# Optimization experiments

Hardware: AMD Instinct MI355X
Metric: run time of the kernel (lower is better)

## Reference

```python
import jax, jax.numpy as jnp
import numpy as np

T, N, E = 4, 50000, 800000
F, H, C_HID, C_OUT = 256, 128, 512, 2
SLOPE = 11.0 / 48.0  # torch RReLU eval-mode slope = (1/8 + 1/3) / 2


def _topk_pool(x, scorer, k):
    # x: [N, d], scorer: [d, 1] -> [d, k]
    scores = (x @ scorer) / jnp.maximum(jnp.linalg.norm(scorer), 1e-6)  # [N, 1]
    _, idx = jax.lax.top_k(scores[:, 0], k)
    return (x[idx] * jnp.tanh(scores[idx])).T


def _gru_cell(prev_Q, z, Wu, Uu, bu, Wr, Ur, br, Wh, Uh, bh):
    u = jax.nn.sigmoid(Wu @ z + Uu @ prev_Q + bu)
    r = jax.nn.sigmoid(Wr @ z + Ur @ prev_Q + br)
    h_cap = jnp.tanh(Wh @ z + Uh @ (r * prev_Q) + bh)
    return (1.0 - u) * prev_Q + u * h_cap


def _gcn_conv(x, src, dst, W):
    ones = jnp.ones(src.shape[0], x.dtype)
    deg_out = jnp.clip(jax.ops.segment_sum(ones, src, num_segments=N), 1.0)
    deg_in = jnp.clip(jax.ops.segment_sum(ones, dst, num_segments=N), 1.0)
    h = (x * (deg_out ** -0.5)[:, None]) @ W          # project first (out <= in)
    agg = jax.ops.segment_sum(h[src], dst, num_segments=N)
    out = agg * (deg_in ** -0.5)[:, None]
    return jnp.where(out >= 0, out, SLOPE * out)      # RReLU (eval mode)


def setup_inputs() -> dict:
    key = jax.random.key(0)
    ks = jax.random.split(key, 32)
    s = 0.05
    d = {}
    d['feats'] = jax.random.normal(ks[0], (T, N, F), jnp.float32)
    d['edges'] = jax.random.randint(ks[1], (T, 2, E), 0, N)
    d['scorer0'] = jax.random.normal(ks[2], (F, 1), jnp.float32) * s
    d['scorer1'] = jax.random.normal(ks[3], (H, 1), jnp.float32) * s
    d['gcn_W0'] = jax.random.normal(ks[4], (F, H), jnp.float32) * s
    d['gcn_W1'] = jax.random.normal(ks[5], (H, H), jnp.float32) * s
    i = 6
    for g in ('u', 'r', 'h'):
        d[g + '_W0'] = jax.random.normal(ks[i], (F, F), jnp.float32) * s; i += 1
        d[g + '_U0'] = jax.random.normal(ks[i], (F, F), jnp.float32) * s; i += 1
        d[g + '_b0'] = jax.random.normal(ks[i], (F, H), jnp.float32) * s; i += 1
    for g in ('u', 'r', 'h'):
        d[g + '_W1'] = jax.random.normal(ks[i], (H, H), jnp.float32) * s; i += 1
        d[g + '_U1'] = jax.random.normal(ks[i], (H, H), jnp.float32) * s; i += 1
        d[g + '_b1'] = jax.random.normal(ks[i], (H, H), jnp.float32) * s; i += 1
    d['mlp_W1'] = jax.random.normal(ks[i], (H, C_HID), jnp.float32) * s; i += 1
    d['mlp_b1'] = jax.random.normal(ks[i], (C_HID,), jnp.float32) * s; i += 1
    d['mlp_W2'] = jax.random.normal(ks[i], (C_HID, C_OUT), jnp.float32) * s; i += 1
    d['mlp_b2'] = jax.random.normal(ks[i], (C_OUT,), jnp.float32) * s
    return d


def reference(feats, edges, scorer0, scorer1, gcn_W0, gcn_W1,
              u_W0, u_U0, u_b0, r_W0, r_U0, r_b0, h_W0, h_U0, h_b0,
              u_W1, u_U1, u_b1, r_W1, r_U1, r_b1, h_W1, h_U1, h_b1,
              mlp_W1, mlp_b1, mlp_W2, mlp_b2):
    feat_list = [feats[t] for t in range(T)]
    scorers = [scorer0, scorer1]
    gcn_Ws = [gcn_W0, gcn_W1]
    grus = [(u_W0, u_U0, u_b0, r_W0, r_U0, r_b0, h_W0, h_U0, h_b0),
            (u_W1, u_U1, u_b1, r_W1, r_U1, r_b1, h_W1, h_U1, h_b1)]
    for i in range(2):
        W = gcn_Ws[i]
        for t in range(T):
            src, dst = edges[t, 0], edges[t, 1]
            X_tilde = _topk_pool(feat_list[t], scorers[i], H)
            W = _gru_cell(W, X_tilde, *grus[i])
            feat_list[t] = _gcn_conv(feat_list[t], src, dst, W)
    x = feat_list[-1]
    x = jnp.maximum(x @ mlp_W1 + mlp_b1, 0.0)
    return x @ mlp_W2 + mlp_b2
```

## Files before the change

kernel.cpp:

```cpp
#include <hip/hip_runtime.h>

#define NT 4
#define NN 50000
#define NE 800000
#define FD 256
#define HD 128
#define CH 512
#define NBINS 4096
#define CAPC 256
#define RSLOPE 0.22916666666666666f

#define NCH 32
#define CHE (NE / NCH)
#define HALFN 25000
#define WPH 12500
#define WPC 25000

#define C_NORM0 0
#define C_NORM1 1

#define SCAN_BLOCKS 49
#define BT0SZ (HD * 2 * FD)
#define BT1SZ (HD * 2 * HD)

typedef __attribute__((ext_vector_type(8))) short bf16x8;
typedef __attribute__((ext_vector_type(4))) float f32x4;

__device__ __forceinline__ float wsumf(float v) {
  for (int m = 32; m > 0; m >>= 1) v += __shfl_xor(v, m, 64);
  return v;
}

__device__ __forceinline__ unsigned short f2bf(float x) {
  unsigned int u = __float_as_uint(x);
  u += 0x7fffu + ((u >> 16) & 1u);
  return (unsigned short)(u >> 16);
}
__device__ __forceinline__ float bf2f(unsigned short h) {
  return __uint_as_float(((unsigned int)h) << 16);
}
__device__ __forceinline__ int sbin(float s) {
  int b = (int)floorf((s + 16.f) * 128.f);
  return max(0, min(NBINS - 1, b));
}

__global__ void k_norm(const float* __restrict__ s, int d, float* ctlf, int slot) {
  __shared__ float red[256];
  float v = ((int)threadIdx.x < d) ? s[threadIdx.x] * s[threadIdx.x] : 0.f;
  red[threadIdx.x] = v;
  __syncthreads();
  for (int o = 128; o > 0; o >>= 1) {
    if ((int)threadIdx.x < o) red[threadIdx.x] += red[threadIdx.x + o];
    __syncthreads();
  }
  if (threadIdx.x == 0) ctlf[slot] = fmaxf(sqrtf(red[0]), 1e-6f);
}

__global__ __launch_bounds__(1024) void k_degC(const int* __restrict__ edges,
                                               unsigned int* __restrict__ chist) {
  __shared__ unsigned int lcnt[WPH];
  int t = blockIdx.y, c = blockIdx.x;
  int tid = threadIdx.x;
  for (int dir = 0; dir < 2; ++dir) {
    const int* E = edges + (size_t)t * 2 * NE + (size_t)dir * NE + (size_t)c * CHE;
    for (int half = 0; half < 2; ++half) {
      for (int i = tid; i < WPH; i += 1024) lcnt[i] = 0;
      __syncthreads();
      int lo = half * HALFN;
      for (int j = tid; j < CHE; j += 1024) {
        int n = E[j] - lo;
        if ((unsigned)n < (unsigned)HALFN)
          atomicAdd(&lcnt[n >> 1], 1u << ((n & 1) * 16));
      }
      __syncthreads();
      unsigned int* dst = chist + (((size_t)dir * NT + t) * NCH + c) * WPC + (size_t)half * WPH;
      for (int i = tid; i < WPH; i += 1024) dst[i] = lcnt[i];
      __syncthreads();
    }
  }
}

__global__ __launch_bounds__(1024) void k_scanB(const unsigned int* __restrict__ chist,
                                                unsigned int* __restrict__ lbase,
                                                float* __restrict__ dor4,
                                                float* __restrict__ din4,
                                                int* __restrict__ rowptr4,
                                                int* __restrict__ bsum4) {
  int t = blockIdx.y;
// ... 76 lines not shown
  const int* rowptr = rowptr4 + (size_t)t * (NN + 1);
  const unsigned int* lb = lbase + ((size_t)t * NCH + c) * NN;
  int* srcs = srcs4 + (size_t)t * NE;
  for (int half = 0; half < 2; ++half) {
    for (int i = tid; i < WPH; i += 1024) lcnt[i] = 0;
    __syncthreads();
    int lo = half * HALFN;
    for (int j = tid; j < CHE; j += 1024) {
      int d = dstE[j];
      int n = d - lo;
      if ((unsigned)n < (unsigned)HALFN) {
        unsigned int old = atomicAdd(&lcnt[n >> 1], 1u << ((n & 1) * 16));
        int ord = (int)((old >> ((n & 1) * 16)) & 0xffff);
        int pos = rowptr[d] + (int)lb[d] + ord;
        srcs[pos] = srcE[j];
      }
    }
    __syncthreads();
  }
}

__global__ void k_scores0_all(const float* __restrict__ feats, const float* __restrict__ sc,
                              const float* __restrict__ ctlf, float* __restrict__ scores0) {
  int t = blockIdx.y;
  int w = (blockIdx.x * blockDim.x + threadIdx.x) >> 6;
  int lane = threadIdx.x & 63;
  if (w >= NN) return;
  size_t rowoff = ((size_t)t * NN + w) * FD;
  float4 x = *(const float4*)(feats + rowoff + lane * 4);
  float4 s = *(const float4*)(sc + lane * 4);
  double acc = (double)x.x * s.x + (double)x.y * s.y + (double)x.z * s.z + (double)x.w * s.w;
  for (int m = 32; m > 0; m >>= 1) acc += __shfl_xor(acc, m, 64);
  if (lane == 0) scores0[(size_t)t * NN + w] = (float)(acc / (double)ctlf[C_NORM0]);
}

__global__ __launch_bounds__(256) void k_cvtT(const float* __restrict__ src, int R, int C,
                                              unsigned short* __restrict__ dhi,
                                              unsigned short* __restrict__ dlo,
                                              int ldd, int roff) {
  __shared__ float t[32][33];
  int bc = blockIdx.x * 32, br = blockIdx.y * 32;
  int lr = threadIdx.x >> 5, lc = threadIdx.x & 31;
#pragma unroll
  for (int q = 0; q < 4; ++q) {
    int r = br + lr + q * 8;
    t[lr + q * 8][lc] = src[(size_t)r * C + bc + lc];
  }
  __syncthreads();
#pragma unroll
  for (int q = 0; q < 4; ++q) {
    int dr = lr + q * 8;
    float v = t[lc][dr];
    unsigned short h = f2bf(v);
    unsigned short l = f2bf(v - bf2f(h));
    size_t o = (size_t)(bc + dr) * ldd + roff + br + lc;
    dhi[o] = h;
    dlo[o] = l;
  }
}

__global__ void k_catsplit(int d, const float* __restrict__ Wu, const float* __restrict__ Uu,
                           const float* __restrict__ Wr, const float* __restrict__ Ur,
                           const float* __restrict__ Wh,
                           unsigned short* __restrict__ hi, unsigned short* __restrict__ lo) {
  int idx = blockIdx.x * 256 + threadIdx.x;
  int K = 2 * d;
  if (idx >= 3 * d * K) return;
  int row = idx / K, col = idx - row * K;
  int reg = row / d;
  int i = row - reg * d;
  float v;
  if (reg == 0) v = (col < d) ? Wu[i * d + col] : Uu[i * d + col - d];
  else if (reg == 1) v = (col < d) ? Wr[i * d + col] : Ur[i * d + col - d];
  else v = (col < d) ? Wh[i * d + col] : 0.f;
  unsigned short h = f2bf(v);
  hi[idx] = h;
  lo[idx] = f2bf(v - bf2f(h));
}

__global__ void k_split(int n, const float* __restrict__ src,
                        unsigned short* __restrict__ hi, unsigned short* __restrict__ lo) {
  int idx = blockIdx.x * 256 + threadIdx.x;
  if (idx >= n) return;
  float v = src[idx];
  unsigned short h = f2bf(v);
  hi[idx] = h;
  lo[idx] = f2bf(v - bf2f(h));
}

template <int LOGD>
__global__ __launch_bounds__(1024) void k_pool(const float* __restrict__ Xb, long xStride,
                                               const float* __restrict__ scoresB, int sStride,
                                               unsigned short* __restrict__ bthiB,
                                               unsigned short* __restrict__ btloB,
                                               long btStride, int ldb) {
  const int D = 1 << LOGD;
  int t = blockIdx.x;
  const float* X = Xb + (size_t)t * xStride;
  const float* scores = scoresB + (size_t)t * sStride;
  unsigned short* bthi = bthiB + (size_t)t * btStride;
  unsigned short* btlo = btloB + (size_t)t * btStride;
  __shared__ int hist[NBINS];
  __shared__ int sufT[1024];
  __shared__ float cs[CAPC];
  __shared__ int ci[CAPC];
  __shared__ float stv[HD];
  __shared__ int sidx[HD];
  __shared__ int thrBin, cnt;
  int tid = threadIdx.x;
  for (int i = tid; i < NBINS; i += 1024) hist[i] = 0;
  if (tid == 0) cnt = 0;
  __syncthreads();
  for (int i = tid; i < NN; i += 1024) atomicAdd(&hist[sbin(scores[i])], 1);
  __syncthreads();

  int h0 = hist[4 * tid + 0], h1 = hist[4 * tid + 1];
  int h2 = hist[4 * tid + 2], h3 = hist[4 * tid + 3];
  int l3 = h3, l2 = h2 + l3, l1 = h1 + l2, l0 = h0 + l1;
  sufT[tid] = l0;
  __syncthreads();
// ... 35 lines not shown
          float si = cs[i], sl = cs[l];
          int di = ci[i], dl = ci[l];
          bool lb = (sl > si) || (sl == si && dl < di);
          bool ib = (si > sl) || (si == sl && di < dl);
          bool dir = ((i & k) == 0);
          if (dir ? lb : ib) {
            cs[i] = sl; cs[l] = si; ci[i] = dl; ci[l] = di;
          }
        }
      }
      __syncthreads();
    }
  }
  if (tid < HD) {
    stv[tid] = tanhf(cs[tid]);
    sidx[tid] = ci[tid];
  }
  __syncthreads();
  for (int e4 = tid * 4; e4 < D * HD; e4 += 1024 * 4) {
    int j = e4 >> LOGD, f = e4 & (D - 1);
    float4 x = *(const float4*)&X[(size_t)sidx[j] * D + f];
    float sv = stv[j];
    x.x *= sv; x.y *= sv; x.z *= sv; x.w *= sv;
    ushort4 h, l;
    h.x = f2bf(x.x); l.x = f2bf(x.x - bf2f(h.x));
    h.y = f2bf(x.y); l.y = f2bf(x.y - bf2f(h.y));
    h.z = f2bf(x.z); l.z = f2bf(x.z - bf2f(h.z));
    h.w = f2bf(x.w); l.w = f2bf(x.w - bf2f(h.w));
    *(ushort4*)&bthi[(size_t)j * ldb + f] = h;
    *(ushort4*)&btlo[(size_t)j * ldb + f] = l;
  }
}

__global__ __launch_bounds__(256) void k_gruA(
    const unsigned short* __restrict__ Ahi, const unsigned short* __restrict__ Alo,
    const unsigned short* __restrict__ Bhi, const unsigned short* __restrict__ Blo,
    int d, const float* __restrict__ bu, const float* __restrict__ br,
    const float* __restrict__ bh, const float* __restrict__ Q,
    float* __restrict__ u, float* __restrict__ hz,
    unsigned short* __restrict__ rqThi, unsigned short* __restrict__ rqTlo) {
  __shared__ unsigned short AshH[64 * 32], AshL[64 * 32];
  __shared__ unsigned short BshH[128 * 32], BshL[128 * 32];
  int K = 2 * d;
  int tid = threadIdx.x;
  int lane = tid & 63, wave = tid >> 6;
  int wr = wave >> 1, wc = wave & 1;
  int n0 = blockIdx.x * 64;
  f32x4 acc[2][4];
#pragma unroll
  for (int m = 0; m < 2; ++m)
#pragma unroll
    for (int n = 0; n < 4; ++n) acc[m][n] = (f32x4){0.f, 0.f, 0.f, 0.f};
  int arow = tid >> 2, aseg = tid & 3;
  int as = (aseg ^ (arow & 3)) * 8;
  int kseg = lane >> 4;
  for (int k0 = 0; k0 < K; k0 += 32) {
    __syncthreads();
    {
      size_t off = (size_t)(n0 + arow) * K + k0 + aseg * 8;
      *(bf16x8*)&AshH[arow * 32 + as] = *(const bf16x8*)(Ahi + off);
      *(bf16x8*)&AshL[arow * 32 + as] = *(const bf16x8*)(Alo + off);
    }
#pragma unroll
    for (int h = 0; h < 2; ++h) {
      int id = tid + h * 256;
      int br2 = id >> 2, bseg = id & 3;
      int bs = (bseg ^ (br2 & 3)) * 8;
      size_t off = (size_t)br2 * K + k0 + bseg * 8;
      *(bf16x8*)&BshH[br2 * 32 + bs] = *(const bf16x8*)(Bhi + off);
      *(bf16x8*)&BshL[br2 * 32 + bs] = *(const bf16x8*)(Blo + off);
    }
    __syncthreads();
    bf16x8 ah[2], al[2], bh8[4], bl8[4];
#pragma unroll
    for (int m = 0; m < 2; ++m) {
      int row = wr * 32 + m * 16 + (lane & 15);
      int s = (kseg ^ (row & 3)) * 8;
      ah[m] = *(bf16x8*)&AshH[row * 32 + s];
      al[m] = *(bf16x8*)&AshL[row * 32 + s];
    }
// ... 10 lines not shown
      for (int n = 0; n < 4; ++n) {
        acc[m][n] = __builtin_amdgcn_mfma_f32_16x16x32_bf16(ah[m], bh8[n], acc[m][n], 0, 0, 0);
        acc[m][n] = __builtin_amdgcn_mfma_f32_16x16x32_bf16(al[m], bh8[n], acc[m][n], 0, 0, 0);
        acc[m][n] = __builtin_amdgcn_mfma_f32_16x16x32_bf16(ah[m], bl8[n], acc[m][n], 0, 0, 0);
      }
  }
  int reg = n0 / d;
#pragma unroll
  for (int m = 0; m < 2; ++m) {
#pragma unroll
    for (int q = 0; q < 4; ++q) {
      int row = n0 + wr * 32 + m * 16 + (lane >> 4) * 4 + q;
      int i = row - reg * d;
#pragma unroll
      for (int n = 0; n < 4; ++n) {
        int col = wc * 64 + n * 16 + (lane & 15);
        float a = acc[m][n][q];
        if (reg == 0) {
          u[i * HD + col] = 1.f / (1.f + expf(-(a + bu[i * HD + col])));
        } else if (reg == 1) {
          float r = 1.f / (1.f + expf(-(a + br[i * HD + col])));
          float rq = r * Q[i * HD + col];
          unsigned short h = f2bf(rq);
          rqThi[(size_t)col * d + i] = h;
          rqTlo[(size_t)col * d + i] = f2bf(rq - bf2f(h));
        } else {
          hz[i * HD + col] = a + bh[i * HD + col];
        }
      }
    }
  }
}

__global__ __launch_bounds__(256) void k_gruB(
    const unsigned short* __restrict__ Ahi, const unsigned short* __restrict__ Alo,
    const unsigned short* __restrict__ Bhi, const unsigned short* __restrict__ Blo,
    int d, const float* __restrict__ hz, const float* __restrict__ u,
    float* __restrict__ Q, unsigned short* __restrict__ BTWhi,
    unsigned short* __restrict__ BTWlo, int ldbt) {
  __shared__ unsigned short AshH[64 * 32], AshL[64 * 32];
  __shared__ unsigned short BshH[128 * 32], BshL[128 * 32];
  int K = d;
  int tid = threadIdx.x;
  int lane = tid & 63, wave = tid >> 6;
  int wr = wave >> 1, wc = wave & 1;
  int n0 = blockIdx.x * 64;
  f32x4 acc[2][4];
#pragma unroll
  for (int m = 0; m < 2; ++m)
#pragma unroll
    for (int n = 0; n < 4; ++n) acc[m][n] = (f32x4){0.f, 0.f, 0.f, 0.f};
  int arow = tid >> 2, aseg = tid & 3;
  int as = (aseg ^ (arow & 3)) * 8;
  int kseg = lane >> 4;
  for (int k0 = 0; k0 < K; k0 += 32) {
    __syncthreads();
    {
      size_t off = (size_t)(n0 + arow) * K + k0 + aseg * 8;
      *(bf16x8*)&AshH[arow * 32 + as] = *(const bf16x8*)(Ahi + off);
      *(bf16x8*)&AshL[arow * 32 + as] = *(const bf16x8*)(Alo + off);
    }
#pragma unroll
    for (int h = 0; h < 2; ++h) {
      int id = tid + h * 256;
      int br2 = id >> 2, bseg = id & 3;
      int bs = (bseg ^ (br2 & 3)) * 8;
      size_t off = (size_t)br2 * K + k0 + bseg * 8;
      *(bf16x8*)&BshH[br2 * 32 + bs] = *(const bf16x8*)(Bhi + off);
      *(bf16x8*)&BshL[br2 * 32 + bs] = *(const bf16x8*)(Blo + off);
    }
    __syncthreads();
    bf16x8 ah[2], al[2], bh8[4], bl8[4];
#pragma unroll
    for (int m = 0; m < 2; ++m) {
      int row = wr * 32 + m * 16 + (lane & 15);
      int s = (kseg ^ (row & 3)) * 8;
      ah[m] = *(bf16x8*)&AshH[row * 32 + s];
      al[m] = *(bf16x8*)&AshL[row * 32 + s];
    }
// ... 1 lines not shown
    for (int n = 0; n < 4; ++n) {
      int col = wc * 64 + n * 16 + (lane & 15);
      int s = (kseg ^ (col & 3)) * 8;
      bh8[n] = *(bf16x8*)&BshH[col * 32 + s];
      bl8[n] = *(bf16x8*)&BshL[col * 32 + s];
    }
#pragma unroll
    for (int m = 0; m < 2; ++m)
#pragma unroll
      for (int n = 0; n < 4; ++n) {
        acc[m][n] = __builtin_amdgcn_mfma_f32_16x16x32_bf16(ah[m], bh8[n], acc[m][n], 0, 0, 0);
        acc[m][n] = __builtin_amdgcn_mfma_f32_16x16x32_bf16(al[m], bh8[n], acc[m][n], 0, 0, 0);
        acc[m][n] = __builtin_amdgcn_mfma_f32_16x16x32_bf16(ah[m], bl8[n], acc[m][n], 0, 0, 0);
      }
  }
#pragma unroll
  for (int m = 0; m < 2; ++m) {
#pragma unroll
    for (int q = 0; q < 4; ++q) {
      int i = n0 + wr * 32 + m * 16 + (lane >> 4) * 4 + q;
#pragma unroll
      for (int n = 0; n < 4; ++n) {
        int col = wc * 64 + n * 16 + (lane & 15);
        float hc = tanhf(acc[m][n][q] + hz[i * HD + col]);
        float uu = u[i * HD + col];
        float qv = Q[i * HD + col];
        float wn = (1.f - uu) * qv + uu * hc;
        Q[i * HD + col] = wn;
        unsigned short h = f2bf(wn);
        BTWhi[(size_t)col * ldbt + i] = h;
        BTWlo[(size_t)col * ldbt + i] = f2bf(wn - bf2f(h));
      }
    }
  }
}

__global__ __launch_bounds__(256) void k_convL0(
    const float* __restrict__ feats,
    const unsigned short* __restrict__ bt0hi, const unsigned short* __restrict__ bt0lo,
    float* __restrict__ C4, const float* __restrict__ dor4) {
  __shared__ unsigned short AshH[64 * 32], AshL[64 * 32];
  __shared__ unsigned short BshH[128 * 32], BshL[128 * 32];
  const int K = FD, ldb = 2 * FD;
  int t = blockIdx.z;
  const float* Af = feats + (size_t)t * NN * FD;
  size_t bOff = (size_t)((t + 1) & 3) * BT0SZ + FD;
  const unsigned short* Bhi = bt0hi + bOff;
  const unsigned short* Blo = bt0lo + bOff;
  float* C = C4 + (size_t)t * NN * HD;
  const float* rs = dor4 + (size_t)t * NN;
  int tid = threadIdx.x;
  int lane = tid & 63, wave = tid >> 6;
  int wr = wave >> 1, wc = wave & 1;
  int n0 = blockIdx.x * 64;
  f32x4 acc[2][4];
#pragma unroll
  for (int m = 0; m < 2; ++m)
#pragma unroll
    for (int n = 0; n < 4; ++n) acc[m][n] = (f32x4){0.f, 0.f, 0.f, 0.f};

  int arow = tid >> 2, aseg = tid & 3;
  int as = (aseg ^ (arow & 3)) * 8;
  int kseg = lane >> 4;

  for (int k0 = 0; k0 < K; k0 += 32) {
    __syncthreads();
// ... 124 lines not shown
#pragma unroll
    for (int n = 0; n < 4; ++n) {
      int col = wc * 64 + n * 16 + (lane & 15);
      int s = (kseg ^ (col & 3)) * 8;
      bh[n] = *(bf16x8*)&BshH[col * 32 + s];
      bl[n] = *(bf16x8*)&BshL[col * 32 + s];
    }
#pragma unroll
    for (int m = 0; m < 2; ++m)
#pragma unroll
      for (int n = 0; n < 4; ++n) {
        acc[m][n] = __builtin_amdgcn_mfma_f32_16x16x32_bf16(ah[m], bh[n], acc[m][n], 0, 0, 0);
        acc[m][n] = __builtin_amdgcn_mfma_f32_16x16x32_bf16(al[m], bh[n], acc[m][n], 0, 0, 0);
        acc[m][n] = __builtin_amdgcn_mfma_f32_16x16x32_bf16(ah[m], bl[n], acc[m][n], 0, 0, 0);
      }
  }

#pragma unroll
  for (int m = 0; m < 2; ++m) {
#pragma unroll
    for (int q = 0; q < 4; ++q) {
      int row = n0 + wr * 32 + m * 16 + (lane >> 4) * 4 + q;
      if (row >= M) continue;
      float rsv = rs[row];
#pragma unroll
      for (int n = 0; n < 4; ++n) {
        int col = c0 + wc * 64 + n * 16 + (lane & 15);
        C[(size_t)row * ldo + col] = acc[m][n][q] * rsv;
      }
    }
  }
}

__global__ __launch_bounds__(256) void k_gemmMLP(
    const unsigned short* __restrict__ Ahi, const unsigned short* __restrict__ Alo,
    const unsigned short* __restrict__ Bhi, const unsigned short* __restrict__ Blo,
    const float* __restrict__ bias, const float* __restrict__ W2,
    const float* __restrict__ b2, float* __restrict__ out, int M) {
  __shared__ unsigned short AshH[64 * 128], AshL[64 * 128];
  __shared__ unsigned short BshH[128 * 32], BshL[128 * 32];
  __shared__ float osum[64][2];
  int tid = threadIdx.x;
  int lane = tid & 63, wave = tid >> 6;
  int wr = wave >> 1, wc = wave & 1;
  int n0 = blockIdx.x * 64;
  if (tid < 128) ((float*)osum)[tid] = 0.f;

  {
    int row = tid >> 2, sq = tid & 3;
    int grow = n0 + row;
#pragma unroll
    for (int q = 0; q < 4; ++q) {
      int s = sq * 4 + q;
      bf16x8 vh = (bf16x8)(short)0, vl = (bf16x8)(short)0;
      if (grow < M) {
        size_t off = (size_t)grow * HD + s * 8;
        vh = *(const bf16x8*)(Ahi + off);
        vl = *(const bf16x8*)(Alo + off);
      }
      int sp = (s ^ (row & 15)) * 8;
      *(bf16x8*)&AshH[row * 128 + sp] = vh;
      *(bf16x8*)&AshL[row * 128 + sp] = vl;
    }
  }
  __syncthreads();

  float ps0[2][4], ps1[2][4];
#pragma unroll
  for (int m = 0; m < 2; ++m)
#pragma unroll
    for (int q = 0; q < 4; ++q) { ps0[m][q] = 0.f; ps1[m][q] = 0.f; }

  int kseg = lane >> 4;
  for (int hc = 0; hc < 4; ++hc) {
    f32x4 acc[2][4];
#pragma unroll
    for (int m = 0; m < 2; ++m)
#pragma unroll
      for (int n = 0; n < 4; ++n) acc[m][n] = (f32x4){0.f, 0.f, 0.f, 0.f};
    for (int k0 = 0; k0 < HD; k0 += 32) {
      __syncthreads();
#pragma unroll
      for (int h = 0; h < 2; ++h) {
        int id = tid + h * 256;
        int br = id >> 2, bseg = id & 3;
        int bs = (bseg ^ (br & 3)) * 8;
        size_t off = (size_t)(hc * 128 + br) * HD + k0 + bseg * 8;
        *(bf16x8*)&BshH[br * 32 + bs] = *(const bf16x8*)(Bhi + off);
        *(bf16x8*)&BshL[br * 32 + bs] = *(const bf16x8*)(Blo + off);
      }
      __syncthreads();
      bf16x8 ah[2], al[2], bh[4], bl[4];
#pragma unroll
      for (int m = 0; m < 2; ++m) {
        int row = wr * 32 + m * 16 + (lane & 15);
        int sg = (k0 >> 3) + kseg;
        int sp = (sg ^ (row & 15)) * 8;
        ah[m] = *(bf16x8*)&AshH[row * 128 + sp];
        al[m] = *(bf16x8*)&AshL[row * 128 + sp];
      }
#pragma unroll
      for (int n = 0; n < 4; ++n) {
        int col = wc * 64 + n * 16 + (lane & 15);
        int s = (kseg ^ (col & 3)) * 8;
        bh[n] = *(bf16x8*)&BshH[col * 32 + s];
        bl[n] = *(bf16x8*)&BshL[col * 32 + s];
      }
#pragma unroll
      for (int m = 0; m < 2; ++m)
#pragma unroll
        for (int n = 0; n < 4; ++n) {
          acc[m][n] = __builtin_amdgcn_mfma_f32_16x16x32_bf16(ah[m], bh[n], acc[m][n], 0, 0, 0);
          acc[m][n] = __builtin_amdgcn_mfma_f32_16x16x32_bf16(al[m], bh[n], acc[m][n], 0, 0, 0);
          acc[m][n] = __builtin_amdgcn_mfma_f32_16x16x32_bf16(ah[m], bl[n], acc[m][n], 0, 0, 0);
        }
    }
#pragma unroll
// ... 62 lines not shown
    float2 v4 = *(const float2*)&h[(size_t)s4 * HD + l2o];
    float2 v5 = *(const float2*)&h[(size_t)s5 * HD + l2o];
    float2 v6 = *(const float2*)&h[(size_t)s6 * HD + l2o];
    float2 v7 = *(const float2*)&h[(size_t)s7 * HD + l2o];
    ax += ((v0.x + v1.x) + (v2.x + v3.x)) + ((v4.x + v5.x) + (v6.x + v7.x));
    ay += ((v0.y + v1.y) + (v2.y + v3.y)) + ((v4.y + v5.y) + (v6.y + v7.y));
  }
  for (; e + 2 <= end; e += 2) {
    int s0 = srcs[e + 0], s1 = srcs[e + 1];
    float2 v0 = *(const float2*)&h[(size_t)s0 * HD + l2o];
    float2 v1 = *(const float2*)&h[(size_t)s1 * HD + l2o];
    ax += v0.x + v1.x;
    ay += v0.y + v1.y;
  }
  for (; e < end; ++e) {
    int s = srcs[e];
    float2 v = *(const float2*)&h[(size_t)s * HD + l2o];
    ax += v.x; ay += v.y;
  }
  float dn = din4[(size_t)t * NN + w];
  ax *= dn; ay *= dn;
  ax = ax >= 0.f ? ax : RSLOPE * ax;
  ay = ay >= 0.f ? ay : RSLOPE * ay;
  *(float2*)&featA4[((size_t)t * NN + w) * HD + l2o] = make_float2(ax, ay);
  if (t == NT - 1) {
    unsigned short hx = f2bf(ax), hy = f2bf(ay);
    unsigned short lx = f2bf(ax - bf2f(hx)), ly = f2bf(ay - bf2f(hy));
    *(ushort2*)&outHi[(size_t)w * HD + l2o] = make_ushort2(hx, hy);
    *(ushort2*)&outLo[(size_t)w * HD + l2o] = make_ushort2(lx, ly);
  }
  float sp = ax * scorer[l2o] + ay * scorer[l2o + 1];
  sp = wsumf(sp);
  if (lane == 0) scores1_4[(size_t)t * NN + w] = sp / ctlf[C_NORM1];
}

__global__ void k_aggF(const float* __restrict__ h, const int* __restrict__ rowptr,
                       const int* __restrict__ srcs, const float* __restrict__ din,
                       unsigned short* __restrict__ outHi, unsigned short* __restrict__ outLo) {
  int w = (blockIdx.x * blockDim.x + threadIdx.x) >> 6;
  int lane = threadIdx.x & 63;
  if (w >= NN) return;
  int beg = rowptr[w], end = rowptr[w + 1];
  float ax = 0.f, ay = 0.f;
  int e = beg;
  int l2o = lane * 2;
  for (; e + 8 <= end; e += 8) {
    int s0 = srcs[e + 0], s1 = srcs[e + 1], s2 = srcs[e + 2], s3 = srcs[e + 3];
    int s4 = srcs[e + 4], s5 = srcs[e + 5], s6 = srcs[e + 6], s7 = srcs[e + 7];
    float2 v0 = *(const float2*)&h[(size_t)s0 * HD + l2o];
    float2 v1 = *(const float2*)&h[(size_t)s1 * HD + l2o];
    float2 v2 = *(const float2*)&h[(size_t)s2 * HD + l2o];
    float2 v3 = *(const float2*)&h[(size_t)s3 * HD + l2o];
    float2 v4 = *(const float2*)&h[(size_t)s4 * HD + l2o];
    float2 v5 = *(const float2*)&h[(size_t)s5 * HD + l2o];
    float2 v6 = *(const float2*)&h[(size_t)s6 * HD + l2o];
    float2 v7 = *(const float2*)&h[(size_t)s7 * HD + l2o];
    ax += ((v0.x + v1.x) + (v2.x + v3.x)) + ((v4.x + v5.x) + (v6.x + v7.x));
    ay += ((v0.y + v1.y) + (v2.y + v3.y)) + ((v4.y + v5.y) + (v6.y + v7.y));
  }
  for (; e + 2 <= end; e += 2) {
    int s0 = srcs[e + 0], s1 = srcs[e + 1];
    float2 v0 = *(const float2*)&h[(size_t)s0 * HD + l2o];
    float2 v1 = *(const float2*)&h[(size_t)s1 * HD + l2o];
    ax += v0.x + v1.x;
    ay += v0.y + v1.y;
  }
  for (; e < end; ++e) {
    int s = srcs[e];
    float2 v = *(const float2*)&h[(size_t)s * HD + l2o];
    ax += v.x; ay += v.y;
  }
  float dn = din[w];
  ax *= dn; ay *= dn;
  ax = ax >= 0.f ? ax : RSLOPE * ax;
  ay = ay >= 0.f ? ay : RSLOPE * ay;
  unsigned short hx = f2bf(ax), hy = f2bf(ay);
  unsigned short lx = f2bf(ax - bf2f(hx)), ly = f2bf(ay - bf2f(hy));
  *(ushort2*)&outHi[(size_t)w * HD + l2o] = make_ushort2(hx, hy);
  *(ushort2*)&outLo[(size_t)w * HD + l2o] = make_ushort2(lx, ly);
}

extern "C" void kernel_launch(void* const* d_in, const int* in_sizes, int n_in,
                              void* d_out, int out_size, void* d_ws, size_t ws_size,
                              hipStream_t stream) {
  (void)in_sizes; (void)n_in; (void)out_size; (void)ws_size;
  const float* feats = (const float*)d_in[0];
  const int* edges = (const int*)d_in[1];
  const float* scorer0 = (const float*)d_in[2];
  const float* scorer1 = (const float*)d_in[3];
  const float* gcnW0 = (const float*)d_in[4];
  const float* gcnW1 = (const float*)d_in[5];
  const float* g0[9];
  const float* g1[9];
  for (int i = 0; i < 9; ++i) {
    g0[i] = (const float*)d_in[6 + i];
    g1[i] = (const float*)d_in[15 + i];
  }
  const float* mlpW1 = (const float*)d_in[24];
  const float* mlpB1 = (const float*)d_in[25];
  const float* mlpW2 = (const float*)d_in[26];
  const float* mlpB2 = (const float*)d_in[27];
  float* out = (float*)d_out;

  char* p = (char*)d_ws;
  auto carve = [&p](size_t bytes) {
    void* r = (void*)p;
    p += (bytes + 511) & ~(size_t)511;
    return r;
  };
  float* featA4 = (float*)carve((size_t)NT * NN * HD * 4);
  float* hbuf4  = (float*)carve((size_t)NT * NN * HD * 4);
  unsigned short* fahi = (unsigned short*)carve((size_t)NN * HD * 2);
  unsigned short* falo = (unsigned short*)carve((size_t)NN * HD * 2);
  int* srcs4   = (int*)carve((size_t)NT * NE * 4);
  int* rowptr4 = (int*)carve((size_t)NT * (NN + 1) * 4);
  unsigned int* chist = (unsigned int*)carve((size_t)2 * NT * NCH * WPC * 4);
  unsigned int* lbase = (unsigned int*)carve((size_t)NT * NCH * NN * 4);
  int* bsum4   = (int*)carve((size_t)NT * SCAN_BLOCKS * 4);
  float* dor4  = (float*)carve((size_t)NT * NN * 4);
  float* din4  = (float*)carve((size_t)NT * NN * 4);
  float* scores0 = (float*)carve((size_t)NT * NN * 4);
  float* scores1_4 = (float*)carve((size_t)NT * NN * 4);
  float* ctlf  = (float*)carve(64 * 4);
  unsigned short* bt0hi = (unsigned short*)carve((size_t)NT * BT0SZ * 2);
  unsigned short* bt0lo = (unsigned short*)carve((size_t)NT * BT0SZ * 2);
  unsigned short* bt1hi = (unsigned short*)carve((size_t)NT * BT1SZ * 2);
  unsigned short* bt1lo = (unsigned short*)carve((size_t)NT * BT1SZ * 2);
  unsigned short* rqThi = (unsigned short*)carve((size_t)HD * FD * 2);
  unsigned short* rqTlo = (unsigned short*)carve((size_t)HD * FD * 2);
  float* ubuf_f = (float*)carve((size_t)FD * HD * 4);
  float* hzbuf  = (float*)carve((size_t)FD * HD * 4);
  unsigned short* acat0hi = (unsigned short*)carve((size_t)3 * FD * 2 * FD * 2);
  unsigned short* acat0lo = (unsigned short*)carve((size_t)3 * FD * 2 * FD * 2);
  unsigned short* acat1hi = (unsigned short*)carve((size_t)3 * HD * 2 * HD * 2);
  unsigned short* acat1lo = (unsigned short*)carve((size_t)3 * HD * 2 * HD * 2);
  unsigned short* uh0hi = (unsigned short*)carve((size_t)FD * FD * 2);
  unsigned short* uh0lo = (unsigned short*)carve((size_t)FD * FD * 2);
  unsigned short* uh1hi = (unsigned short*)carve((size_t)HD * HD * 2);
  unsigned short* uh1lo = (unsigned short*)carve((size_t)HD * HD * 2);
  float* Q0 = (float*)carve((size_t)FD * HD * 4);
  float* Q1 = (float*)carve((size_t)HD * HD * 4);
  unsigned short* mW1thi = (unsigned short*)carve((size_t)CH * HD * 2);
  unsigned short* mW1tlo = (unsigned short*)carve((size_t)CH * HD * 2);

  hipMemcpyAsync(Q0, gcnW0, (size_t)FD * HD * 4, hipMemcpyDeviceToDevice, stream);
  hipMemcpyAsync(Q1, gcnW1, (size_t)HD * HD * 4, hipMemcpyDeviceToDevice, stream);
  k_norm<<<1, 256, 0, stream>>>(scorer0, FD, ctlf, C_NORM0);
  k_norm<<<1, 256, 0, stream>>>(scorer1, HD, ctlf, C_NORM1);
  k_cvtT<<<dim3(CH / 32, HD / 32), 256, 0, stream>>>(mlpW1, HD, CH, mW1thi, mW1tlo, HD, 0);
  k_cvtT<<<dim3(HD / 32, FD / 32), 256, 0, stream>>>(gcnW0, FD, HD, bt0hi, bt0lo, 2 * FD, FD);
  k_cvtT<<<dim3(HD / 32, HD / 32), 256, 0, stream>>>(gcnW1, HD, HD, bt1hi, bt1lo, 2 * HD, HD);
  k_catsplit<<<(3 * FD * 2 * FD + 255) / 256, 256, 0, stream>>>(FD, g0[0], g0[1], g0[3], g0[4], g0[6], acat0hi, acat0lo);
  k_catsplit<<<(3 * HD * 2 * HD + 255) / 256, 256, 0, stream>>>(HD, g1[0], g1[1], g1[3], g1[4], g1[6], acat1hi, acat1lo);
  k_split<<<(FD * FD + 255) / 256, 256, 0, stream>>>(FD * FD, g0[7], uh0hi, uh0lo);
  k_split<<<(HD * HD + 255) / 256, 256, 0, stream>>>(HD * HD, g1[7], uh1hi, uh1lo);

  k_scores0_all<<<dim3(12500, NT), 256, 0, stream>>>(feats, scorer0, ctlf, scores0);
  k_degC<<<dim3(NCH, NT), 1024, 0, stream>>>(edges, chist);
  k_scanB<<<dim3(SCAN_BLOCKS, NT), 1024, 0, stream>>>(chist, lbase, dor4, din4, rowptr4, bsum4);
  k_scan2b<<<NT, 1024, 0, stream>>>(rowptr4, bsum4);
  k_scatC<<<dim3(NCH, NT), 1024, 0, stream>>>(edges, rowptr4, lbase, srcs4);
  k_pool<8><<<NT, 1024, 0, stream>>>(feats, (long)NN * FD, scores0, NN,
                                     bt0hi, bt0lo, (long)BT0SZ, 2 * FD);

  for (int t = 0; t < NT; ++t) {
    size_t btOff = (size_t)t * BT0SZ;
    size_t btNxt = (size_t)((t + 1) & 3) * BT0SZ;
    k_gruA<<<3 * FD / 64, 256, 0, stream>>>(acat0hi, acat0lo, bt0hi + btOff, bt0lo + btOff,
                                            FD, g0[2], g0[5], g0[8], Q0, ubuf_f, hzbuf,
                                            rqThi, rqTlo);
    k_gruB<<<FD / 64, 256, 0, stream>>>(uh0hi, uh0lo, rqThi, rqTlo, FD, hzbuf, ubuf_f, Q0,
                                        bt0hi + btNxt + FD, bt0lo + btNxt + FD, 2 * FD);
  }

  const int gM = (NN + 63) / 64;

  k_convL0<<<dim3(gM, 1, NT), 256, 0, stream>>>(feats, bt0hi, bt0lo, hbuf4, dor4);

  k_aggB<<<dim3(12500, NT), 256, 0, stream>>>(hbuf4, rowptr4, srcs4, din4, featA4,
                                              scorer1, ctlf, scores1_4, fahi, falo);

  k_pool<7><<<NT, 1024, 0, stream>>>(featA4, (long)NN * HD, scores1_4, NN,
                                     bt1hi, bt1lo, (long)BT1SZ, 2 * HD);

  for (int t = 0; t < NT; ++t) {
    size_t btOff = (size_t)t * BT1SZ;
    size_t btNxt = (size_t)((t + 1) & 3) * BT1SZ;
    k_gruA<<<3 * HD / 64, 256, 0, stream>>>(acat1hi, acat1lo, bt1hi + btOff, bt1lo + btOff,
                                            HD, g1[2], g1[5], g1[8], Q1, ubuf_f, hzbuf,
                                            rqThi, rqTlo);
    k_gruB<<<HD / 64, 256, 0, stream>>>(uh1hi, uh1lo, rqThi, rqTlo, HD, hzbuf, ubuf_f, Q1,
                                        bt1hi + btNxt + HD, bt1lo + btNxt + HD, 2 * HD);
  }

  k_gemm3<<<dim3(gM, 1), 256, 0, stream>>>(fahi, falo, HD,
                                           bt1hi + HD, bt1lo + HD, 2 * HD,
                                           hbuf4, HD, NN, HD, dor4 + (size_t)3 * NN);
  k_aggF<<<12500, 256, 0, stream>>>(hbuf4, rowptr4 + (size_t)3 * (NN + 1),
                                    srcs4 + (size_t)3 * NE, din4 + (size_t)3 * NN,
                                    fahi, falo);
  k_gemmMLP<<<gM, 256, 0, stream>>>(fahi, falo, mW1thi, mW1tlo, mlpB1, mlpW2, mlpB2, out, NN);
}
```

Measured before the change: 1.089 ms.

## Merge setup kernels, run GRU chain persistently with grid barriers, fuse final aggregation into MLP

The separate setup launches and two memcpys are merged into a single k_startup kernel that dispatches on block index. Each GRU time loop is now one persistent kernel that uses a global atomic barrier between the gruA and gruB phases, replacing eight small launches per layer. The final edge aggregation is folded into the MLP GEMM's A-tile load, so the bf16 feature round trip through memory is gone. The risks are that the spin barrier assumes all blocks are co-resident, and that aggregation with one thread per 32-column segment may gather less efficiently than the old wave-per-row layout.

```diff
diff --git a/kernel.cpp b/kernel.cpp
--- a/kernel.cpp
+++ b/kernel.cpp
@@ -23,6 +23,20 @@
 #define BT0SZ (HD * 2 * FD)
 #define BT1SZ (HD * 2 * HD)
 
+#define SU_NORM0 0
+#define SU_NORM1 1
+#define SU_CVT_A 2
+#define SU_CVT_B 66
+#define SU_CVT_C 98
+#define SU_CAT0 114
+#define SU_CAT1 1650
+#define SU_SPL0 2034
+#define SU_SPL1 2290
+#define SU_CPQ0 2354
+#define SU_CPQ1 2386
+#define SU_ZBAR 2402
+#define SU_TOTAL 2403
+
 typedef __attribute__((ext_vector_type(8))) short bf16x8;
 typedef __attribute__((ext_vector_type(4))) float f32x4;
 
@@ -44,8 +58,20 @@
   return max(0, min(NBINS - 1, b));
 }
 
-__global__ void k_norm(const float* __restrict__ s, int d, float* ctlf, int slot) {
-  __shared__ float red[256];
+__device__ __forceinline__ void gbar(unsigned int* bar, int nblk, int gen) {
+  __syncthreads();
+  if (threadIdx.x == 0) {
+    __threadfence();
+    atomicAdd(bar, 1u);
+    unsigned int tgt = (unsigned int)(nblk * (gen + 1));
+    while (atomicAdd(bar, 0u) < tgt) __builtin_amdgcn_s_sleep(2);
+    __threadfence();
+  }
+  __syncthreads();
+}
+
+__device__ __forceinline__ void d_norm(const float* s, int d, float* ctlf, int slot,
+                                       float* red) {
   float v = ((int)threadIdx.x < d) ? s[threadIdx.x] * s[threadIdx.x] : 0.f;
   red[threadIdx.x] = v;
   __syncthreads();
@@ -54,6 +80,102 @@
     __syncthreads();
   }
   if (threadIdx.x == 0) ctlf[slot] = fmaxf(sqrtf(red[0]), 1e-6f);
+}
+
+__device__ __forceinline__ void d_cvtT(int bx, int by, const float* __restrict__ src, int C,
+                                       unsigned short* __restrict__ dhi,
+                                       unsigned short* __restrict__ dlo,
+                                       int ldd, int roff, float (*t)[33]) {
+  int bc = bx * 32, br = by * 32;
+  int lr = threadIdx.x >> 5, lc = threadIdx.x & 31;
+#pragma unroll
+  for (int q = 0; q < 4; ++q) {
+    int r = br + lr + q * 8;
+    t[lr + q * 8][lc] = src[(size_t)r * C + bc + lc];
+  }
+  __syncthreads();
+#pragma unroll
+  for (int q = 0; q < 4; ++q) {
+    int dr = lr + q * 8;
+    float v = t[lc][dr];
+    unsigned short h = f2bf(v);
+    unsigned short l = f2bf(v - bf2f(h));
+    size_t o = (size_t)(bc + dr) * ldd + roff + br + lc;
+    dhi[o] = h;
+    dlo[o] = l;
+  }
+}
+
+__device__ __forceinline__ void d_catsplit(int blk, int d, const float* __restrict__ Wu,
+                                           const float* __restrict__ Uu,
+                                           const float* __restrict__ Wr,
+                                           const float* __restrict__ Ur,
+                                           const float* __restrict__ Wh,
+                                           unsigned short* __restrict__ hi,
+                                           unsigned short* __restrict__ lo) {
+  int idx = blk * 256 + threadIdx.x;
+  int K = 2 * d;
+  if (idx >= 3 * d * K) return;
+  int row = idx / K, col = idx - row * K;
+  int reg = row / d;
+  int i = row - reg * d;
+  float v;
+  if (reg == 0) v = (col < d) ? Wu[i * d + col] : Uu[i * d + col - d];
+  else if (reg == 1) v = (col < d) ? Wr[i * d + col] : Ur[i * d + col - d];
+  else v = (col < d) ? Wh[i * d + col] : 0.f;
+  unsigned short h = f2bf(v);
+  hi[idx] = h;
+  lo[idx] = f2bf(v - bf2f(h));
+}
+
+__device__ __forceinline__ void d_split(int blk, int n, const float* __restrict__ src,
+                                        unsigned short* __restrict__ hi,
+                                        unsigned short* __restrict__ lo) {
+  int idx = blk * 256 + threadIdx.x;
+  if (idx >= n) return;
+  float v = src[idx];
+  unsigned short h = f2bf(v);
+  hi[idx] = h;
+  lo[idx] = f2bf(v - bf2f(h));
+}
+
+__global__ __launch_bounds__(256) void k_startup(
+    const float* __restrict__ scorer0, const float* __restrict__ scorer1,
+    float* __restrict__ ctlf,
+    const float* __restrict__ mlpW1, unsigned short* __restrict__ mW1thi,
+    unsigned short* __restrict__ mW1tlo,
+    const float* __restrict__ gcnW0, const float* __restrict__ gcnW1,
+    unsigned short* __restrict__ bt0hi, unsigned short* __restrict__ bt0lo,
+    unsigned short* __restrict__ bt1hi, unsigned short* __restrict__ bt1lo,
+    const float* __restrict__ u_W0, const float* __restrict__ u_U0,
+    const float* __restrict__ r_W0, const float* __restrict__ r_U0,
+    const float* __restrict__ h_W0,
+    unsigned short* __restrict__ acat0hi, unsigned short* __restrict__ acat0lo,
+    const float* __restrict__ u_W1, const float* __restrict__ u_U1,
+    const float* __restrict__ r_W1, const float* __restrict__ r_U1,
+    const float* __restrict__ h_W1,
+    unsigned short* __restrict__ acat1hi, unsigned short* __restrict__ acat1lo,
+    const float* __restrict__ uh0, unsigned short* __restrict__ uh0hi,
+    unsigned short* __restrict__ uh0lo,
+    const float* __restrict__ uh1, unsigned short* __restrict__ uh1hi,
+    unsigned short* __restrict__ uh1lo,
+    float* __restrict__ Q0, float* __restrict__ Q1,
+    unsigned int* __restrict__ bar) {
+  __shared__ float red[256];
+  __shared__ float tile[32][33];
+  int b = blockIdx.x;
+  if (b == SU_NORM0) { d_norm(scorer0, FD, ctlf, C_NORM0, red); return; }
+  if (b == SU_NORM1) { d_norm(scorer1, HD, ctlf, C_NORM1, red); return; }
+  if (b < SU_CVT_B) { int r = b - SU_CVT_A; d_cvtT(r & 15, r >> 4, mlpW1, CH, mW1thi, mW1tlo, HD, 0, tile); return; }
+  if (b < SU_CVT_C) { int r = b - SU_CVT_B; d_cvtT(r & 3, r >> 2, gcnW0, HD, bt0hi, bt0lo, 2 * FD, FD, tile); return; }
+  if (b < SU_CAT0)  { int r = b - SU_CVT_C; d_cvtT(r & 3, r >> 2, gcnW1, HD, bt1hi, bt1lo, 2 * HD, HD, tile); return; }
+  if (b < SU_CAT1)  { d_catsplit(b - SU_CAT0, FD, u_W0, u_U0, r_W0, r_U0, h_W0, acat0hi, acat0lo); return; }
+  if (b < SU_SPL0)  { d_catsplit(b - SU_CAT1, HD, u_W1, u_U1, r_W1, r_U1, h_W1, acat1hi, acat1lo); return; }
+  if (b < SU_SPL1)  { d_split(b - SU_SPL0, FD * FD, uh0, uh0hi, uh0lo); return; }
+  if (b < SU_CPQ0)  { d_split(b - SU_SPL1, HD * HD, uh1, uh1hi, uh1lo); return; }
+  if (b < SU_CPQ1)  { int i = (b - SU_CPQ0) * 256 + threadIdx.x; ((float4*)Q0)[i] = ((const float4*)gcnW0)[i]; return; }
+  if (b < SU_ZBAR)  { int i = (b - SU_CPQ1) * 256 + threadIdx.x; ((float4*)Q1)[i] = ((const float4*)gcnW1)[i]; return; }
+  if (threadIdx.x < 16) bar[threadIdx.x] = 0;
 }
 
 __global__ __launch_bounds__(1024) void k_degC(const int* __restrict__ edges,
@@ -196,60 +318,6 @@
   double acc = (double)x.x * s.x + (double)x.y * s.y + (double)x.z * s.z + (double)x.w * s.w;
   for (int m = 32; m > 0; m >>= 1) acc += __shfl_xor(acc, m, 64);
   if (lane == 0) scores0[(size_t)t * NN + w] = (float)(acc / (double)ctlf[C_NORM0]);
-}
-
-__global__ __launch_bounds__(256) void k_cvtT(const float* __restrict__ src, int R, int C,
-                                              unsigned short* __restrict__ dhi,
-                                              unsigned short* __restrict__ dlo,
-                                              int ldd, int roff) {
-  __shared__ float t[32][33];
-  int bc = blockIdx.x * 32, br = blockIdx.y * 32;
-  int lr = threadIdx.x >> 5, lc = threadIdx.x & 31;
-#pragma unroll
-  for (int q = 0; q < 4; ++q) {
-    int r = br + lr + q * 8;
-    t[lr + q * 8][lc] = src[(size_t)r * C + bc + lc];
-  }
-  __syncthreads();
-#pragma unroll
-  for (int q = 0; q < 4; ++q) {
-    int dr = lr + q * 8;
-    float v = t[lc][dr];
-    unsigned short h = f2bf(v);
-    unsigned short l = f2bf(v - bf2f(h));
-    size_t o = (size_t)(bc + dr) * ldd + roff + br + lc;
-    dhi[o] = h;
-    dlo[o] = l;
-  }
-}
-
-__global__ void k_catsplit(int d, const float* __restrict__ Wu, const float* __restrict__ Uu,
-                           const float* __restrict__ Wr, const float* __restrict__ Ur,
-                           const float* __restrict__ Wh,
-                           unsigned short* __restrict__ hi, unsigned short* __restrict__ lo) {
-  int idx = blockIdx.x * 256 + threadIdx.x;
-  int K = 2 * d;
-  if (idx >= 3 * d * K) return;
-  int row = idx / K, col = idx - row * K;
-  int reg = row / d;
-  int i = row - reg * d;
-  float v;
-  if (reg == 0) v = (col < d) ? Wu[i * d + col] : Uu[i * d + col - d];
-  else if (reg == 1) v = (col < d) ? Wr[i * d + col] : Ur[i * d + col - d];
-  else v = (col < d) ? Wh[i * d + col] : 0.f;
-  unsigned short h = f2bf(v);
-  hi[idx] = h;
-  lo[idx] = f2bf(v - bf2f(h));
-}
-
-__global__ void k_split(int n, const float* __restrict__ src,
-                        unsigned short* __restrict__ hi, unsigned short* __restrict__ lo) {
-  int idx = blockIdx.x * 256 + threadIdx.x;
-  if (idx >= n) return;
-  float v = src[idx];
-  unsigned short h = f2bf(v);
-  hi[idx] = h;
-  lo[idx] = f2bf(v - bf2f(h));
 }
 
 template <int LOGD>
@@ -351,20 +419,20 @@
   }
 }
 
-__global__ __launch_bounds__(256) void k_gruA(
-    const unsigned short* __restrict__ Ahi, const unsigned short* __restrict__ Alo,
+__device__ __forceinline__ void gruA_body(
+    int bx, const unsigned short* __restrict__ Ahi, const unsigned short* __restrict__ Alo,
     const unsigned short* __restrict__ Bhi, const unsigned short* __restrict__ Blo,
     int d, const float* __restrict__ bu, const float* __restrict__ br,
     const float* __restrict__ bh, const float* __restrict__ Q,
     float* __restrict__ u, float* __restrict__ hz,
-    unsigned short* __restrict__ rqThi, unsigned short* __restrict__ rqTlo) {
-  __shared__ unsigned short AshH[64 * 32], AshL[64 * 32];
-  __shared__ unsigned short BshH[128 * 32], BshL[128 * 32];
+    unsigned short* __restrict__ rqThi, unsigned short* __restrict__ rqTlo,
+    unsigned short* AshH, unsigned short* AshL,
+    unsigned short* BshH, unsigned short* BshL) {
   int K = 2 * d;
   int tid = threadIdx.x;
   int lane = tid & 63, wave = tid >> 6;
   int wr = wave >> 1, wc = wave & 1;
-  int n0 = blockIdx.x * 64;
+  int n0 = bx * 64;
   f32x4 acc[2][4];
 #pragma unroll
   for (int m = 0; m < 2; ++m)
@@ -441,19 +509,19 @@
   }
 }
 
-__global__ __launch_bounds__(256) void k_gruB(
-    const unsigned short* __restrict__ Ahi, const unsigned short* __restrict__ Alo,
+__device__ __forceinline__ void gruB_body(
+    int bx, const unsigned short* __restrict__ Ahi, const unsigned short* __restrict__ Alo,
     const unsigned short* __restrict__ Bhi, const unsigned short* __restrict__ Blo,
     int d, const float* __restrict__ hz, const float* __restrict__ u,
     float* __restrict__ Q, unsigned short* __restrict__ BTWhi,
-    unsigned short* __restrict__ BTWlo, int ldbt) {
-  __shared__ unsigned short AshH[64 * 32], AshL[64 * 32];
-  __shared__ unsigned short BshH[128 * 32], BshL[128 * 32];
+    unsigned short* __restrict__ BTWlo, int ldbt,
+    unsigned short* AshH, unsigned short* AshL,
+    unsigned short* BshH, unsigned short* BshL) {
   int K = d;
   int tid = threadIdx.x;
   int lane = tid & 63, wave = tid >> 6;
   int wr = wave >> 1, wc = wave & 1;
-  int n0 = blockIdx.x * 64;
+  int n0 = bx * 64;
   f32x4 acc[2][4];
 #pragma unroll
   for (int m = 0; m < 2; ++m)
@@ -521,6 +589,34 @@
         BTWlo[(size_t)col * ldbt + i] = f2bf(wn - bf2f(h));
       }
     }
+  }
+}
+
+__global__ __launch_bounds__(256) void k_gruChain(
+    const unsigned short* __restrict__ Ahi, const unsigned short* __restrict__ Alo,
+    unsigned short* __restrict__ bthi, unsigned short* __restrict__ btlo, long btSz,
+    int d, const float* __restrict__ gb_u, const float* __restrict__ gb_r,
+    const float* __restrict__ gb_h, float* __restrict__ Q,
+    float* __restrict__ ubuf, float* __restrict__ hzbuf,
+    unsigned short* __restrict__ rqThi, unsigned short* __restrict__ rqTlo,
+    const unsigned short* __restrict__ uhhi, const unsigned short* __restrict__ uhlo,
+    unsigned int* bar) {
+  __shared__ unsigned short AshH[64 * 32], AshL[64 * 32];
+  __shared__ unsigned short BshH[128 * 32], BshL[128 * 32];
+  int nb = (int)gridDim.x;
+  for (int t = 0; t < NT; ++t) {
+    gruA_body((int)blockIdx.x, Ahi, Alo,
+              bthi + (size_t)t * btSz, btlo + (size_t)t * btSz, d,
+              gb_u, gb_r, gb_h, Q, ubuf, hzbuf, rqThi, rqTlo,
+              AshH, AshL, BshH, BshL);
+    gbar(bar, nb, 2 * t);
+    if ((int)blockIdx.x < (d >> 6)) {
+      size_t nxt = (size_t)((t + 1) & 3) * btSz;
+      gruB_body((int)blockIdx.x, uhhi, uhlo, rqThi, rqTlo, d, hzbuf, ubuf, Q,
+                bthi + nxt + d, btlo + nxt + d, 2 * d,
+                AshH, AshL, BshH, BshL);
+    }
+    if (t < NT - 1) gbar(bar, nb, 2 * t + 1);
   }
 }
 
@@ -711,8 +807,9 @@
   }
 }
 
-__global__ __launch_bounds__(256) void k_gemmMLP(
-    const unsigned short* __restrict__ Ahi, const unsigned short* __restrict__ Alo,
+__global__ __launch_bounds__(256) void k_gemmMLPagg(
+    const float* __restrict__ h, const int* __restrict__ rowptr,
+    const int* __restrict__ srcs, const float* __restrict__ din,
     const unsigned short* __restrict__ Bhi, const unsigned short* __restrict__ Blo,
     const float* __restrict__ bias, const float* __restrict__ W2,
     const float* __restrict__ b2, float* __restrict__ out, int M) {
@@ -726,16 +823,40 @@
   if (tid < 128) ((float*)osum)[tid] = 0.f;
 
   {
-    int row = tid >> 2, sq = tid & 3;
+    int row = tid >> 2, seg = tid & 3;
     int grow = n0 + row;
+    float a[32];
+#pragma unroll
+    for (int i = 0; i < 32; ++i) a[i] = 0.f;
+    if (grow < M) {
+      int beg = rowptr[grow], end = rowptr[grow + 1];
+      int c0 = seg * 32;
+      for (int e = beg; e < end; ++e) {
+        const float* hr = h + (size_t)srcs[e] * HD + c0;
+#pragma unroll
+        for (int i = 0; i < 8; ++i) {
+          float4 v = *(const float4*)(hr + i * 4);
+          a[i * 4 + 0] += v.x; a[i * 4 + 1] += v.y;
+          a[i * 4 + 2] += v.z; a[i * 4 + 3] += v.w;
+        }
+      }
+      float dn = din[grow];
+#pragma unroll
+      for (int i = 0; i < 32; ++i) {
+        float v = a[i] * dn;
+        a[i] = v >= 0.f ? v : RSLOPE * v;
+      }
+    }
 #pragma unroll
     for (int q = 0; q < 4; ++q) {
-      int s = sq * 4 + q;
-      bf16x8 vh = (bf16x8)(short)0, vl = (bf16x8)(short)0;
-      if (grow < M) {
-        size_t off = (size_t)grow * HD + s * 8;
-        vh = *(const bf16x8*)(Ahi + off);
-        vl = *(const bf16x8*)(Alo + off);
+      int s = seg * 4 + q;
+      bf16x8 vh, vl;
+#pragma unroll
+      for (int j = 0; j < 8; ++j) {
+        float v = a[q * 8 + j];
+        unsigned short hh = f2bf(v);
+        vh[j] = (short)hh;
+        vl[j] = (short)f2bf(v - bf2f(hh));
       }
       int sp = (s ^ (row & 15)) * 8;
       *(bf16x8*)&AshH[row * 128 + sp] = vh;
@@ -760,8 +881,8 @@
     for (int k0 = 0; k0 < HD; k0 += 32) {
       __syncthreads();
 #pragma unroll
-      for (int h = 0; h < 2; ++h) {
-        int id = tid + h * 256;
+      for (int h2 = 0; h2 < 2; ++h2) {
+        int id = tid + h2 * 256;
         int br = id >> 2, bseg = id & 3;
         int bs = (bseg ^ (br & 3)) * 8;
         size_t off = (size_t)(hc * 128 + br) * HD + k0 + bseg * 8;
@@ -890,52 +1011,6 @@
   float sp = ax * scorer[l2o] + ay * scorer[l2o + 1];
   sp = wsumf(sp);
   if (lane == 0) scores1_4[(size_t)t * NN + w] = sp / ctlf[C_NORM1];
-}
-
-__global__ void k_aggF(const float* __restrict__ h, const int* __restrict__ rowptr,
-                       const int* __restrict__ srcs, const float* __restrict__ din,
-                       unsigned short* __restrict__ outHi, unsigned short* __restrict__ outLo) {
-  int w = (blockIdx.x * blockDim.x + threadIdx.x) >> 6;
-  int lane = threadIdx.x & 63;
-  if (w >= NN) return;
-  int beg = rowptr[w], end = rowptr[w + 1];
-  float ax = 0.f, ay = 0.f;
-  int e = beg;
-  int l2o = lane * 2;
-  for (; e + 8 <= end; e += 8) {
-    int s0 = srcs[e + 0], s1 = srcs[e + 1], s2 = srcs[e + 2], s3 = srcs[e + 3];
-    int s4 = srcs[e + 4], s5 = srcs[e + 5], s6 = srcs[e + 6], s7 = srcs[e + 7];
-    float2 v0 = *(const float2*)&h[(size_t)s0 * HD + l2o];
-    float2 v1 = *(const float2*)&h[(size_t)s1 * HD + l2o];
-    float2 v2 = *(const float2*)&h[(size_t)s2 * HD + l2o];
-    float2 v3 = *(const float2*)&h[(size_t)s3 * HD + l2o];
-    float2 v4 = *(const float2*)&h[(size_t)s4 * HD + l2o];
-    float2 v5 = *(const float2*)&h[(size_t)s5 * HD + l2o];
-    float2 v6 = *(const float2*)&h[(size_t)s6 * HD + l2o];
-    float2 v7 = *(const float2*)&h[(size_t)s7 * HD + l2o];
-    ax += ((v0.x + v1.x) + (v2.x + v3.x)) + ((v4.x + v5.x) + (v6.x + v7.x));
-    ay += ((v0.y + v1.y) + (v2.y + v3.y)) + ((v4.y + v5.y) + (v6.y + v7.y));
-  }
-  for (; e + 2 <= end; e += 2) {
-    int s0 = srcs[e + 0], s1 = srcs[e + 1];
-    float2 v0 = *(const float2*)&h[(size_t)s0 * HD + l2o];
-    float2 v1 = *(const float2*)&h[(size_t)s1 * HD + l2o];
-    ax += v0.x + v1.x;
-    ay += v0.y + v1.y;
-  }
-  for (; e < end; ++e) {
-    int s = srcs[e];
-    float2 v = *(const float2*)&h[(size_t)s * HD + l2o];
-    ax += v.x; ay += v.y;
-  }
-  float dn = din[w];
-  ax *= dn; ay *= dn;
-  ax = ax >= 0.f ? ax : RSLOPE * ax;
-  ay = ay >= 0.f ? ay : RSLOPE * ay;
-  unsigned short hx = f2bf(ax), hy = f2bf(ay);
-  unsigned short lx = f2bf(ax - bf2f(hx)), ly = f2bf(ay - bf2f(hy));
-  *(ushort2*)&outHi[(size_t)w * HD + l2o] = make_ushort2(hx, hy);
-  *(ushort2*)&outLo[(size_t)w * HD + l2o] = make_ushort2(lx, ly);
 }
 
 extern "C" void kernel_launch(void* const* d_in, const int* in_sizes, int n_in,
@@ -1000,18 +1075,14 @@
   float* Q1 = (float*)carve((size_t)HD * HD * 4);
   unsigned short* mW1thi = (unsigned short*)carve((size_t)CH * HD * 2);
   unsigned short* mW1tlo = (unsigned short*)carve((size_t)CH * HD * 2);
-
-  hipMemcpyAsync(Q0, gcnW0, (size_t)FD * HD * 4, hipMemcpyDeviceToDevice, stream);
-  hipMemcpyAsync(Q1, gcnW1, (size_t)HD * HD * 4, hipMemcpyDeviceToDevice, stream);
-  k_norm<<<1, 256, 0, stream>>>(scorer0, FD, ctlf, C_NORM0);
-  k_norm<<<1, 256, 0, stream>>>(scorer1, HD, ctlf, C_NORM1);
-  k_cvtT<<<dim3(CH / 32, HD / 32), 256, 0, stream>>>(mlpW1, HD, CH, mW1thi, mW1tlo, HD, 0);
-  k_cvtT<<<dim3(HD / 32, FD / 32), 256, 0, stream>>>(gcnW0, FD, HD, bt0hi, bt0lo, 2 * FD, FD);
-  k_cvtT<<<dim3(HD / 32, HD / 32), 256, 0, stream>>>(gcnW1, HD, HD, bt1hi, bt1lo, 2 * HD, HD);
-  k_catsplit<<<(3 * FD * 2 * FD + 255) / 256, 256, 0, stream>>>(FD, g0[0], g0[1], g0[3], g0[4], g0[6], acat0hi, acat0lo);
-  k_catsplit<<<(3 * HD * 2 * HD + 255) / 256, 256, 0, stream>>>(HD, g1[0], g1[1], g1[3], g1[4], g1[6], acat1hi, acat1lo);
-  k_split<<<(FD * FD + 255) / 256, 256, 0, stream>>>(FD * FD, g0[7], uh0hi, uh0lo);
-  k_split<<<(HD * HD + 255) / 256, 256, 0, stream>>>(HD * HD, g1[7], uh1hi, uh1lo);
+  unsigned int* barbuf = (unsigned int*)carve(64 * 4);
+
+  k_startup<<<SU_TOTAL, 256, 0, stream>>>(
+      scorer0, scorer1, ctlf, mlpW1, mW1thi, mW1tlo, gcnW0, gcnW1,
+      bt0hi, bt0lo, bt1hi, bt1lo,
+      g0[0], g0[1], g0[3], g0[4], g0[6], acat0hi, acat0lo,
+      g1[0], g1[1], g1[3], g1[4], g1[6], acat1hi, acat1lo,
+      g0[7], uh0hi, uh0lo, g1[7], uh1hi, uh1lo, Q0, Q1, barbuf);
 
   k_scores0_all<<<dim3(12500, NT), 256, 0, stream>>>(feats, scorer0, ctlf, scores0);
   k_degC<<<dim3(NCH, NT), 1024, 0, stream>>>(edges, chist);
@@ -1021,15 +1092,10 @@
   k_pool<8><<<NT, 1024, 0, stream>>>(feats, (long)NN * FD, scores0, NN,
                                      bt0hi, bt0lo, (long)BT0SZ, 2 * FD);
 
-  for (int t = 0; t < NT; ++t) {
-    size_t btOff = (size_t)t * BT0SZ;
-    size_t btNxt = (size_t)((t + 1) & 3) * BT0SZ;
-    k_gruA<<<3 * FD / 64, 256, 0, stream>>>(acat0hi, acat0lo, bt0hi + btOff, bt0lo + btOff,
-                                            FD, g0[2], g0[5], g0[8], Q0, ubuf_f, hzbuf,
-                                            rqThi, rqTlo);
-    k_gruB<<<FD / 64, 256, 0, stream>>>(uh0hi, uh0lo, rqThi, rqTlo, FD, hzbuf, ubuf_f, Q0,
-                                        bt0hi + btNxt + FD, bt0lo + btNxt + FD, 2 * FD);
-  }
+  k_gruChain<<<3 * FD / 64, 256, 0, stream>>>(
+      acat0hi, acat0lo, bt0hi, bt0lo, (long)BT0SZ, FD,
+      g0[2], g0[5], g0[8], Q0, ubuf_f, hzbuf, rqThi, rqTlo,
+      uh0hi, uh0lo, barbuf + 0);
 
   const int gM = (NN + 63) / 64;
 
@@ -1041,21 +1107,15 @@
   k_pool<7><<<NT, 1024, 0, stream>>>(featA4, (long)NN * HD, scores1_4, NN,
                                      bt1hi, bt1lo, (long)BT1SZ, 2 * HD);
 
-  for (int t = 0; t < NT; ++t) {
-    size_t btOff = (size_t)t * BT1SZ;
-    size_t btNxt = (size_t)((t + 1) & 3) * BT1SZ;
-    k_gruA<<<3 * HD / 64, 256, 0, stream>>>(acat1hi, acat1lo, bt1hi + btOff, bt1lo + btOff,
-                                            HD, g1[2], g1[5], g1[8], Q1, ubuf_f, hzbuf,
-                                            rqThi, rqTlo);
-    k_gruB<<<HD / 64, 256, 0, stream>>>(uh1hi, uh1lo, rqThi, rqTlo, HD, hzbuf, ubuf_f, Q1,
-                                        bt1hi + btNxt + HD, bt1lo + btNxt + HD, 2 * HD);
-  }
+  k_gruChain<<<3 * HD / 64, 256, 0, stream>>>(
+      acat1hi, acat1lo, bt1hi, bt1lo, (long)BT1SZ, HD,
+      g1[2], g1[5], g1[8], Q1, ubuf_f, hzbuf, rqThi, rqTlo,
+      uh1hi, uh1lo, barbuf + 1);
 
   k_gemm3<<<dim3(gM, 1), 256, 0, stream>>>(fahi, falo, HD,
                                            bt1hi + HD, bt1lo + HD, 2 * HD,
                                            hbuf4, HD, NN, HD, dor4 + (size_t)3 * NN);
-  k_aggF<<<12500, 256, 0, stream>>>(hbuf4, rowptr4 + (size_t)3 * (NN + 1),
-                                    srcs4 + (size_t)3 * NE, din4 + (size_t)3 * NN,
-                                    fahi, falo);
-  k_gemmMLP<<<gM, 256, 0, stream>>>(fahi, falo, mW1thi, mW1tlo, mlpB1, mlpW2, mlpB2, out, NN);
-}
+  k_gemmMLPagg<<<gM, 256, 0, stream>>>(hbuf4, rowptr4 + (size_t)3 * (NN + 1),
+                                       srcs4 + (size_t)3 * NE, din4 + (size_t)3 * NN,
+                                       mW1thi, mW1tlo, mlpB1, mlpW2, mlpB2, out, NN);
+}
```

After: 1.126 ms. +3.3%, slower.
